# Kernel optimization log

Measured on AMD Instinct MI355X. Metric: run time of the kernel, lower is better.

The kernel has to match this reference:

```python
import jax, jax.numpy as jnp
import numpy as np

NUM_EMBEDDINGS = 8192
EMBEDDING_DIM = 256
BETA = 0.25


def setup_inputs() -> dict:
    key = jax.random.key(0)
    k1, k2 = jax.random.split(key)
    z = jax.random.normal(k1, (16, 256, 32, 32), dtype=jnp.float32)
    # nn.Embedding weight init: uniform(-1/K, 1/K)
    emb = jax.random.uniform(k2, (NUM_EMBEDDINGS, EMBEDDING_DIM), dtype=jnp.float32,
                             minval=-1.0 / NUM_EMBEDDINGS, maxval=1.0 / NUM_EMBEDDINGS)
    return {"z": z, "emb": emb}


def reference(z, emb):
    b, c, h, w = z.shape
    flat = z.transpose(0, 2, 3, 1).reshape(-1, c)  # [B*H*W, C]
    distances = (jnp.sum(flat * flat, axis=1, keepdims=True)
                 - 2.0 * flat @ emb.T
                 + jnp.sum(emb * emb, axis=1))  # [B*H*W, K]
    indices = jnp.argmin(distances, axis=1)  # [B*H*W]
    quantized = emb[indices].reshape(b, h, w, c).transpose(0, 3, 1, 2)  # [B,C,H,W]
    codebook_loss = jnp.mean((jax.lax.stop_gradient(quantized) - z) ** 2)
    commitment_loss = BETA * jnp.mean((quantized - jax.lax.stop_gradient(z)) ** 2)
    quantized_st = z + jax.lax.stop_gradient(quantized - z)  # straight-through
    return quantized_st, codebook_loss, commitment_loss, indices.reshape(b, h, w)
```

## Files before the change

kernel.cpp:

```cpp
#include <hip/hip_runtime.h>

#define NROWS   16384
#define KCODES  8192
#define CDIM    256
#define HWS     1024
#define BSTRIDE 262144

#define WS_AN   0
#define WS_CE   16384
#define WS_CD   24576
#define WS_CI   155648
#define WS_IDX  286720
#define WS_LOSS 303104

typedef float f32x2 __attribute__((ext_vector_type(2)));
typedef float f32x4 __attribute__((ext_vector_type(4)));

#define PKFMA_LO(acc, a, b) \
  asm("v_pk_fma_f32 %0, %1, %2, %0 op_sel:[0,0,0] op_sel_hi:[0,1,1]" \
      : "+v"(acc) : "v"(a), "v"(b))
#define PKFMA_HI(acc, a, b) \
  asm("v_pk_fma_f32 %0, %1, %2, %0 op_sel:[1,0,0] op_sel_hi:[1,1,1]" \
      : "+v"(acc) : "v"(a), "v"(b))

__global__ void rownorm_z_k(const float* __restrict__ z, float* __restrict__ An) {
#pragma clang fp contract(off)
  int n = blockIdx.x * 256 + threadIdx.x;
  const float* base = z + ((size_t)(n >> 10)) * BSTRIDE + (n & 1023);
  float hs[2];
  for (int h = 0; h < 2; ++h) {
    float r[8];
#pragma unroll
    for (int j = 0; j < 8; ++j) { float v = base[(size_t)(h * 128 + j) * HWS]; r[j] = v * v; }
    for (int m = 1; m < 16; ++m) {
#pragma unroll
      for (int j = 0; j < 8; ++j) { float v = base[(size_t)(h * 128 + m * 8 + j) * HWS]; r[j] += v * v; }
    }
    hs[h] = ((r[0] + r[1]) + (r[2] + r[3])) + ((r[4] + r[5]) + (r[6] + r[7]));
  }
  An[n] = hs[0] + hs[1];
}

__global__ void rownorm_e_k(const float* __restrict__ emb, float* __restrict__ Ce) {
#pragma clang fp contract(off)
  int n = blockIdx.x * 256 + threadIdx.x;
  const float* base = emb + (size_t)n * CDIM;
  float hs[2];
  for (int h = 0; h < 2; ++h) {
    float r[8];
#pragma unroll
    for (int j = 0; j < 8; ++j) { float v = base[h * 128 + j]; r[j] = v * v; }
    for (int m = 1; m < 16; ++m) {
#pragma unroll
      for (int j = 0; j < 8; ++j) { float v = base[h * 128 + m * 8 + j]; r[j] += v * v; }
    }
    hs[h] = ((r[0] + r[1]) + (r[2] + r[3])) + ((r[4] + r[5]) + (r[6] + r[7]));
  }
  Ce[n] = hs[0] + hs[1];
}

__global__ void __launch_bounds__(256, 2)
vq_argmin_k(const float* __restrict__ z, const float* __restrict__ emb,
            const float* __restrict__ An, const float* __restrict__ Ce,
            float* __restrict__ cand_d, int* __restrict__ cand_i) {
  __shared__ float smem[12288];
  float* As = smem;
  float* Bs = smem + 4096;

  const int t  = threadIdx.x;
  const int tx = t & 15;
  const int ty = t >> 4;
  const int bid   = blockIdx.x;
  const int slice = bid & 7;
  const int tile  = bid >> 3;
  const int rbase = tile * 128;
  const int k0    = slice * 1024;

  const float* zb = z + ((size_t)(rbase >> 10)) * BSTRIDE + (rbase & 1023);

  float best[8];
  int   bidx[8];
#pragma unroll
  for (int ri = 0; ri < 8; ++ri) { best[ri] = 3.4028235e38f; bidx[ri] = 0; }

  f32x2 acc2[8][8];
#pragma unroll
  for (int ri = 0; ri < 8; ++ri)
#pragma unroll
    for (int j = 0; j < 8; ++j) acc2[ri][j] = (f32x2){0.f, 0.f};

  const int a_c   = t >> 4;
  const int a_hw  = (t & 15) * 8;
  const int a_swr = (t & 15) & 7;
  const int a_wi  = a_c & 3;
  const int a_kg1 = a_c >> 2;
  const int acol1 = ((a_kg1 ^ a_swr) << 2) | a_wi;
  const int acol2 = (((a_kg1 + 4) ^ a_swr) << 2) | a_wi;
  const int b_code = t >> 1;
  const int b_cb   = (t & 1) * 16;
  const int b_p    = ((b_code >> 5) << 4) | (b_code & 15);
  const int b_s    = (b_code >> 4) & 1;
  const int b_p7   = b_code & 7;
  const int b_base = b_p * 64 + ((b_cb >> 1) << 2) + b_s;

  const int rd_a_sw = ty & 7;
  const int rd_b_sw = tx & 7;
  const int bB      = tx * 64;

  for (int kc = 0; kc < 4; ++kc) {
    const int kbase = k0 + kc * 256;
#pragma unroll 1
    for (int sc = 0; sc < 8; ++sc) {
      const float* zsrc = zb + (size_t)(sc * 32 + a_c) * HWS + a_hw;
      const float4 pa0 = *(const float4*)(zsrc);
      const float4 pa1 = *(const float4*)(zsrc + 4);
      const float4 pa2 = *(const float4*)(zsrc + 16 * HWS);
      const float4 pa3 = *(const float4*)(zsrc + 16 * HWS + 4);
      const float* bsrc0 = emb + (size_t)(kbase + b_code) * CDIM + sc * 32 + b_cb;
      const float* bsrc1 = bsrc0 + (size_t)128 * CDIM;
      const float4 pb0 = *(const float4*)(bsrc0);
      const float4 pb1 = *(const float4*)(bsrc0 + 4);
      const float4 pb2 = *(const float4*)(bsrc0 + 8);
      const float4 pb3 = *(const float4*)(bsrc0 + 12);
      const float4 pb4 = *(const float4*)(bsrc1);
      const float4 pb5 = *(const float4*)(bsrc1 + 4);
      const float4 pb6 = *(const float4*)(bsrc1 + 8);
      const float4 pb7 = *(const float4*)(bsrc1 + 12);

      __syncthreads();
      {
        const float va0[8] = {pa0.x, pa0.y, pa0.z, pa0.w, pa1.x, pa1.y, pa1.z, pa1.w};
        const float va1[8] = {pa2.x, pa2.y, pa2.z, pa2.w, pa3.x, pa3.y, pa3.z, pa3.w};
#pragma unroll
        for (int j = 0; j < 8; ++j) {
          const int rb = (a_hw + j) << 5;
          As[rb + acol1] = va0[j];
          As[rb + acol2] = va1[j];
        }
        const float bval0[16] = {pb0.x, pb0.y, pb0.z, pb0.w,
                                 pb1.x, pb1.y, pb1.z, pb1.w,
                                 pb2.x, pb2.y, pb2.z, pb2.w,
                                 pb3.x, pb3.y, pb3.z, pb3.w};
        const float bval1[16] = {pb4.x, pb4.y, pb4.z, pb4.w,
                                 pb5.x, pb5.y, pb5.z, pb5.w,
                                 pb6.x, pb6.y, pb6.z, pb6.w,
                                 pb7.x, pb7.y, pb7.z, pb7.w};
#pragma unroll
        for (int i = 0; i < 8; ++i) {
          const int off = b_base + ((i ^ b_p7) << 2);
          Bs[off]            = bval0[2 * i];
          Bs[off + 2]        = bval0[2 * i + 1];
          Bs[off + 4096]     = bval1[2 * i];
          Bs[off + 4096 + 2] = bval1[2 * i + 1];
        }
      }
      __syncthreads();

#pragma unroll
      for (int g = 0; g < 8; ++g) {
        f32x4 av[8];
#pragma unroll
        for (int ri = 0; ri < 8; ++ri)
          av[ri] = *(const f32x4*)&As[((ty * 8 + ri) << 5) + ((g ^ rd_a_sw) << 2)];
        const int sw0 = ((2 * g) ^ rd_b_sw) << 2;
        const int sw1 = sw0 ^ 4;
#pragma unroll
        for (int ci2 = 0; ci2 < 8; ++ci2) {
          const f32x4 b0 = *(const f32x4*)&Bs[bB + ci2 * 1024 + sw0];
          const f32x4 b1 = *(const f32x4*)&Bs[bB + ci2 * 1024 + sw1];
          const f32x2 bk0 = __builtin_shufflevector(b0, b0, 0, 1);
          const f32x2 bk1 = __builtin_shufflevector(b0, b0, 2, 3);
          const f32x2 bk2 = __builtin_shufflevector(b1, b1, 0, 1);
          const f32x2 bk3 = __builtin_shufflevector(b1, b1, 2, 3);
#pragma unroll
          for (int ri = 0; ri < 8; ++ri) {
            const f32x2 a01 = __builtin_shufflevector(av[ri], av[ri], 0, 1);
            const f32x2 a23 = __builtin_shufflevector(av[ri], av[ri], 2, 3);
            PKFMA_HI(acc2[ri][ci2], a23, bk3);
            PKFMA_LO(acc2[ri][ci2], a23, bk2);
            PKFMA_HI(acc2[ri][ci2], a01, bk1);
            PKFMA_LO(acc2[ri][ci2], a01, bk0);
          }
        }
      }
    }

    {
      const int kkb = kbase + tx;
      float cearr[16];
#pragma unroll
      for (int ci = 0; ci < 16; ++ci) cearr[ci] = Ce[kkb + ci * 16];
#pragma unroll
      for (int ri = 0; ri < 8; ++ri) {
        const float Ar = An[rbase + ty * 8 + ri];
#pragma unroll
        for (int ci2 = 0; ci2 < 8; ++ci2) {
          const float d0 = (Ar - 2.0f * acc2[ri][ci2].x) + cearr[2 * ci2];
          if (d0 < best[ri]) { best[ri] = d0; bidx[ri] = kkb + ci2 * 32; }
          const float d1 = (Ar - 2.0f * acc2[ri][ci2].y) + cearr[2 * ci2 + 1];
          if (d1 < best[ri]) { best[ri] = d1; bidx[ri] = kkb + ci2 * 32 + 16; }
          acc2[ri][ci2] = (f32x2){0.f, 0.f};
        }
      }
    }
  }

  __syncthreads();
  float* redd = smem;
  int*   redi = (int*)(smem + 2048);
#pragma unroll
  for (int ri = 0; ri < 8; ++ri) {
    redd[(ty * 8 + ri) * 16 + tx] = best[ri];
    redi[(ty * 8 + ri) * 16 + tx] = bidx[ri];
  }
  __syncthreads();
  if (t < 128) {
    float bd = redd[t * 16];
    int   bi = redi[t * 16];
    for (int j = 1; j < 16; ++j) {
      const float d  = redd[t * 16 + j];
      const int   i2 = redi[t * 16 + j];
      if (d < bd || (d == bd && i2 < bi)) { bd = d; bi = i2; }
    }
    const int n = rbase + t;
    cand_d[n * 8 + slice] = bd;
    cand_i[n * 8 + slice] = bi;
  }
}

__global__ void vq_merge_k(const float* __restrict__ cand_d, const int* __restrict__ cand_i,
                           int* __restrict__ idx_final, float* __restrict__ idxf_out) {
  const int n = blockIdx.x * 256 + threadIdx.x;
  float bd = cand_d[n * 8];
  int   bi = cand_i[n * 8];
#pragma unroll
  for (int s = 1; s < 8; ++s) {
    const float d  = cand_d[n * 8 + s];
    const int   i2 = cand_i[n * 8 + s];
    if (d < bd || (d == bd && i2 < bi)) { bd = d; bi = i2; }
  }
  idx_final[n] = bi;
  idxf_out[n] = (float)bi;
}

__launch_bounds__(256)
__global__ void vq_gather_loss_k(const float* __restrict__ z, const float* __restrict__ emb,
                                 const int* __restrict__ idx_final,
                                 float* __restrict__ qout, float* __restrict__ loss_acc) {
  __shared__ float Qs[32 * 260];
  __shared__ int   kidx[32];
  __shared__ float warp_s[4];
  const int t = threadIdx.x;
  const int rbase = blockIdx.x * 32;
  if (t < 32) kidx[t] = idx_final[rbase + t];
  __syncthreads();
  {
    const int r = t >> 3, cp = t & 7;
    const float4* er = (const float4*)(emb + (size_t)kidx[r] * CDIM);
#pragma unroll
    for (int j = 0; j < 8; ++j) {
      const int c4 = cp + j * 8;
      const float4 v = er[c4];
      *(float4*)&Qs[r * 260 + c4 * 4] = v;
    }
  }
  __syncthreads();
  const int b = rbase >> 10, hw0 = rbase & 1023;
  const float* zb = z + (size_t)b * BSTRIDE + hw0;
  float* qb = qout + (size_t)b * BSTRIDE + hw0;
  float s = 0.f;
  const int hwl = t & 31, cg = t >> 5;
  for (int i = 0; i < 32; ++i) {
    const int c = cg * 32 + i;
    const float q  = Qs[hwl * 260 + c];
    const size_t off = (size_t)c * HWS + hwl;
    const float zv = zb[off];
    const float d  = q - zv;
    qb[off] = zv + d;
    s += d * d;
  }
  for (int off = 32; off; off >>= 1) s += __shfl_down(s, off, 64);
  if ((t & 63) == 0) warp_s[t >> 6] = s;
  __syncthreads();
  if (t == 0) atomicAdd(loss_acc, warp_s[0] + warp_s[1] + warp_s[2] + warp_s[3]);
}

__global__ void vq_finalize_k(const float* __restrict__ loss_acc, float* __restrict__ out_loss) {
  const float m = loss_acc[0] * (1.0f / 4194304.0f);
  out_loss[0] = m;
  out_loss[1] = 0.25f * m;
}

extern "C" void kernel_launch(void* const* d_in, const int* in_sizes, int n_in,
                              void* d_out, int out_size, void* d_ws, size_t ws_size,
                              hipStream_t stream) {
  (void)in_sizes; (void)n_in; (void)out_size; (void)ws_size;
  const float* z   = (const float*)d_in[0];
  const float* emb = (const float*)d_in[1];
  float* out      = (float*)d_out;
  float* q_out    = out;
  float* loss_out = out + 4194304;
  float* idxf_out = out + 4194306;

  float* ws       = (float*)d_ws;
  float* An       = ws + WS_AN;
  float* Ce       = ws + WS_CE;
  float* cand_d   = ws + WS_CD;
  int*   cand_i   = (int*)(ws + WS_CI);
  int*   idx_fin  = (int*)(ws + WS_IDX);
  float* loss_acc = ws + WS_LOSS;

  hipMemsetAsync(loss_acc, 0, sizeof(float), stream);
  rownorm_z_k<<<64, 256, 0, stream>>>(z, An);
  rownorm_e_k<<<32, 256, 0, stream>>>(emb, Ce);
  vq_argmin_k<<<1024, 256, 0, stream>>>(z, emb, An, Ce, cand_d, cand_i);
  vq_merge_k<<<64, 256, 0, stream>>>(cand_d, cand_i, idx_fin, idxf_out);
  vq_gather_loss_k<<<512, 256, 0, stream>>>(z, emb, idx_fin, q_out, loss_acc);
  vq_finalize_k<<<1, 1, 0, stream>>>(loss_acc, loss_out);
}
```

Measured before the change: 889.2 us.

## Split argmin block code tile across two thread halves to halve per-thread accumulators

Doubles the argmin kernel's block size to 512 threads. Each half of the block now handles 128 of the 256 codes in a tile, so each thread holds an 8x4 accumulator instead of 8x8. The global-to-shared load work is spread over twice as many threads, and the final reduction now merges 32 partial minima per row instead of 16. The aim is lower register pressure and higher occupancy, which should hide LDS and global latency better. The cost is more A-tile reads from shared memory per FMA and more threads competing at each barrier.

```diff
diff --git a/kernel.cpp b/kernel.cpp
--- a/kernel.cpp
+++ b/kernel.cpp
@@ -59,7 +59,7 @@
   Ce[n] = hs[0] + hs[1];
 }
 
-__global__ void __launch_bounds__(256, 2)
+__global__ void __launch_bounds__(512, 4)
 vq_argmin_k(const float* __restrict__ z, const float* __restrict__ emb,
             const float* __restrict__ An, const float* __restrict__ Ce,
             float* __restrict__ cand_d, int* __restrict__ cand_i) {
@@ -69,7 +69,8 @@
 
   const int t  = threadIdx.x;
   const int tx = t & 15;
-  const int ty = t >> 4;
+  const int ty = (t >> 4) & 15;
+  const int wz = t >> 8;
   const int bid   = blockIdx.x;
   const int slice = bid & 7;
   const int tile  = bid >> 3;
@@ -83,29 +84,27 @@
 #pragma unroll
   for (int ri = 0; ri < 8; ++ri) { best[ri] = 3.4028235e38f; bidx[ri] = 0; }
 
-  f32x2 acc2[8][8];
+  f32x2 acc2[8][4];
 #pragma unroll
   for (int ri = 0; ri < 8; ++ri)
 #pragma unroll
-    for (int j = 0; j < 8; ++j) acc2[ri][j] = (f32x2){0.f, 0.f};
+    for (int j = 0; j < 4; ++j) acc2[ri][j] = (f32x2){0.f, 0.f};
 
   const int a_c   = t >> 4;
   const int a_hw  = (t & 15) * 8;
   const int a_swr = (t & 15) & 7;
-  const int a_wi  = a_c & 3;
-  const int a_kg1 = a_c >> 2;
-  const int acol1 = ((a_kg1 ^ a_swr) << 2) | a_wi;
-  const int acol2 = (((a_kg1 + 4) ^ a_swr) << 2) | a_wi;
-  const int b_code = t >> 1;
-  const int b_cb   = (t & 1) * 16;
+  const int acol  = (((a_c >> 2) ^ a_swr) << 2) | (a_c & 3);
+  const int b_code = t >> 2;
+  const int b_cb   = (t & 3) * 8;
   const int b_p    = ((b_code >> 5) << 4) | (b_code & 15);
   const int b_s    = (b_code >> 4) & 1;
   const int b_p7   = b_code & 7;
-  const int b_base = b_p * 64 + ((b_cb >> 1) << 2) + b_s;
+  const int b_g0   = b_cb >> 1;
+  const int b_rowb = b_p * 64 + b_s;
 
   const int rd_a_sw = ty & 7;
   const int rd_b_sw = tx & 7;
-  const int bB      = tx * 64;
+  const int bBw     = tx * 64 + wz * 4096;
 
   for (int kc = 0; kc < 4; ++kc) {
     const int kbase = k0 + kc * 256;
@@ -114,40 +113,25 @@
       const float* zsrc = zb + (size_t)(sc * 32 + a_c) * HWS + a_hw;
       const float4 pa0 = *(const float4*)(zsrc);
       const float4 pa1 = *(const float4*)(zsrc + 4);
-      const float4 pa2 = *(const float4*)(zsrc + 16 * HWS);
-      const float4 pa3 = *(const float4*)(zsrc + 16 * HWS + 4);
       const float* bsrc0 = emb + (size_t)(kbase + b_code) * CDIM + sc * 32 + b_cb;
       const float* bsrc1 = bsrc0 + (size_t)128 * CDIM;
       const float4 pb0 = *(const float4*)(bsrc0);
       const float4 pb1 = *(const float4*)(bsrc0 + 4);
-      const float4 pb2 = *(const float4*)(bsrc0 + 8);
-      const float4 pb3 = *(const float4*)(bsrc0 + 12);
-      const float4 pb4 = *(const float4*)(bsrc1);
-      const float4 pb5 = *(const float4*)(bsrc1 + 4);
-      const float4 pb6 = *(const float4*)(bsrc1 + 8);
-      const float4 pb7 = *(const float4*)(bsrc1 + 12);
+      const float4 pb2 = *(const float4*)(bsrc1);
+      const float4 pb3 = *(const float4*)(bsrc1 + 4);
 
       __syncthreads();
       {
-        const float va0[8] = {pa0.x, pa0.y, pa0.z, pa0.w, pa1.x, pa1.y, pa1.z, pa1.w};
-        const float va1[8] = {pa2.x, pa2.y, pa2.z, pa2.w, pa3.x, pa3.y, pa3.z, pa3.w};
+        const float va[8] = {pa0.x, pa0.y, pa0.z, pa0.w, pa1.x, pa1.y, pa1.z, pa1.w};
 #pragma unroll
         for (int j = 0; j < 8; ++j) {
-          const int rb = (a_hw + j) << 5;
-          As[rb + acol1] = va0[j];
-          As[rb + acol2] = va1[j];
+          As[((a_hw + j) << 5) + acol] = va[j];
         }
-        const float bval0[16] = {pb0.x, pb0.y, pb0.z, pb0.w,
-                                 pb1.x, pb1.y, pb1.z, pb1.w,
-                                 pb2.x, pb2.y, pb2.z, pb2.w,
-                                 pb3.x, pb3.y, pb3.z, pb3.w};
-        const float bval1[16] = {pb4.x, pb4.y, pb4.z, pb4.w,
-                                 pb5.x, pb5.y, pb5.z, pb5.w,
-                                 pb6.x, pb6.y, pb6.z, pb6.w,
-                                 pb7.x, pb7.y, pb7.z, pb7.w};
-#pragma unroll
-        for (int i = 0; i < 8; ++i) {
-          const int off = b_base + ((i ^ b_p7) << 2);
+        const float bval0[8] = {pb0.x, pb0.y, pb0.z, pb0.w, pb1.x, pb1.y, pb1.z, pb1.w};
+        const float bval1[8] = {pb2.x, pb2.y, pb2.z, pb2.w, pb3.x, pb3.y, pb3.z, pb3.w};
+#pragma unroll
+        for (int i = 0; i < 4; ++i) {
+          const int off = b_rowb + (((b_g0 + i) ^ b_p7) << 2);
           Bs[off]            = bval0[2 * i];
           Bs[off + 2]        = bval0[2 * i + 1];
           Bs[off + 4096]     = bval1[2 * i];
@@ -165,9 +149,9 @@
         const int sw0 = ((2 * g) ^ rd_b_sw) << 2;
         const int sw1 = sw0 ^ 4;
 #pragma unroll
-        for (int ci2 = 0; ci2 < 8; ++ci2) {
-          const f32x4 b0 = *(const f32x4*)&Bs[bB + ci2 * 1024 + sw0];
-          const f32x4 b1 = *(const f32x4*)&Bs[bB + ci2 * 1024 + sw1];
+        for (int ci2 = 0; ci2 < 4; ++ci2) {
+          const f32x4 b0 = *(const f32x4*)&Bs[bBw + ci2 * 1024 + sw0];
+          const f32x4 b1 = *(const f32x4*)&Bs[bBw + ci2 * 1024 + sw1];
           const f32x2 bk0 = __builtin_shufflevector(b0, b0, 0, 1);
           const f32x2 bk1 = __builtin_shufflevector(b0, b0, 2, 3);
           const f32x2 bk2 = __builtin_shufflevector(b1, b1, 0, 1);
@@ -186,15 +170,18 @@
     }
 
     {
-      const int kkb = kbase + tx;
-      float cearr[16];
-#pragma unroll
-      for (int ci = 0; ci < 16; ++ci) cearr[ci] = Ce[kkb + ci * 16];
+      const int kkb = kbase + tx + 128 * wz;
+      float cearr[8];
+#pragma unroll
+      for (int ci2 = 0; ci2 < 4; ++ci2) {
+        cearr[2 * ci2]     = Ce[kkb + ci2 * 32];
+        cearr[2 * ci2 + 1] = Ce[kkb + ci2 * 32 + 16];
+      }
 #pragma unroll
       for (int ri = 0; ri < 8; ++ri) {
         const float Ar = An[rbase + ty * 8 + ri];
 #pragma unroll
-        for (int ci2 = 0; ci2 < 8; ++ci2) {
+        for (int ci2 = 0; ci2 < 4; ++ci2) {
           const float d0 = (Ar - 2.0f * acc2[ri][ci2].x) + cearr[2 * ci2];
           if (d0 < best[ri]) { best[ri] = d0; bidx[ri] = kkb + ci2 * 32; }
           const float d1 = (Ar - 2.0f * acc2[ri][ci2].y) + cearr[2 * ci2 + 1];
@@ -207,19 +194,19 @@
 
   __syncthreads();
   float* redd = smem;
-  int*   redi = (int*)(smem + 2048);
+  int*   redi = (int*)(smem + 4096);
 #pragma unroll
   for (int ri = 0; ri < 8; ++ri) {
-    redd[(ty * 8 + ri) * 16 + tx] = best[ri];
-    redi[(ty * 8 + ri) * 16 + tx] = bidx[ri];
+    redd[(ty * 8 + ri) * 32 + (wz * 16 + tx)] = best[ri];
+    redi[(ty * 8 + ri) * 32 + (wz * 16 + tx)] = bidx[ri];
   }
   __syncthreads();
   if (t < 128) {
-    float bd = redd[t * 16];
-    int   bi = redi[t * 16];
-    for (int j = 1; j < 16; ++j) {
-      const float d  = redd[t * 16 + j];
-      const int   i2 = redi[t * 16 + j];
+    float bd = redd[t * 32];
+    int   bi = redi[t * 32];
+    for (int j = 1; j < 32; ++j) {
+      const float d  = redd[t * 32 + j];
+      const int   i2 = redi[t * 32 + j];
       if (d < bd || (d == bd && i2 < bi)) { bd = d; bi = i2; }
     }
     const int n = rbase + t;
@@ -313,7 +300,7 @@
   hipMemsetAsync(loss_acc, 0, sizeof(float), stream);
   rownorm_z_k<<<64, 256, 0, stream>>>(z, An);
   rownorm_e_k<<<32, 256, 0, stream>>>(emb, Ce);
-  vq_argmin_k<<<1024, 256, 0, stream>>>(z, emb, An, Ce, cand_d, cand_i);
+  vq_argmin_k<<<1024, 512, 0, stream>>>(z, emb, An, Ce, cand_d, cand_i);
   vq_merge_k<<<64, 256, 0, stream>>>(cand_d, cand_i, idx_fin, idxf_out);
   vq_gather_loss_k<<<512, 256, 0, stream>>>(z, emb, idx_fin, q_out, loss_acc);
   vq_finalize_k<<<1, 1, 0, stream>>>(loss_acc, loss_out);
```

Measured after the change: 975.9 us. 1.1x slower.
